# Kernel optimization log

Measured on AMD Instinct MI355X. Metric: run time of the kernel, lower is better.

Reference implementation:

```python
import jax, jax.numpy as jnp
import numpy as np

H, W = 480, 640
N = 256
CFEAT = 256
FAR = 80.0

def _quat_to_rot(q):
    # q: [N,4] normalized (w,x,y,z)
    w, x, y, z = q[:, 0], q[:, 1], q[:, 2], q[:, 3]
    return jnp.stack([
        jnp.stack([1 - 2 * (y * y + z * z), 2 * (x * y - w * z), 2 * (x * z + w * y)], -1),
        jnp.stack([2 * (x * y + w * z), 1 - 2 * (x * x + z * z), 2 * (y * z - w * x)], -1),
        jnp.stack([2 * (x * z - w * y), 2 * (y * z + w * x), 1 - 2 * (x * x + y * y)], -1)], -2)

def setup_inputs():
    key = jax.random.key(0)
    ks = jax.random.split(key, 10)
    z = jax.random.uniform(ks[0], (N,), minval=2.0, maxval=30.0)
    x = jax.random.uniform(ks[1], (N,), minval=-0.6, maxval=0.6) * z
    y = jax.random.uniform(ks[2], (N,), minval=-0.45, maxval=0.45) * z
    means3d = jnp.stack([x, y, z], -1)                                   # [N,3] in front of camera
    features = jax.random.normal(ks[3], (N, CFEAT))                      # [N,256]
    opacities = jax.random.uniform(ks[4], (N,), minval=0.3, maxval=0.95)
    scales = jax.random.uniform(ks[5], (N, 3), minval=0.05, maxval=0.4)
    rotations = jax.random.normal(ks[6], (N, 4))                         # unnormalized quats
    cam_K = jnp.array([[500.0, 0.0, 320.0], [0.0, 500.0, 240.0], [0.0, 0.0, 1.0]])
    cam_pose = jnp.eye(4)
    w1 = jax.random.normal(ks[7], (CFEAT, 128)) * (1.0 / np.sqrt(CFEAT))
    b1 = jnp.zeros((128,))
    w2 = jax.random.normal(ks[8], (128, 128)) * (1.0 / np.sqrt(128))
    b2 = jnp.zeros((128,))
    w3 = jax.random.normal(ks[9], (128, 12)) * (1.0 / np.sqrt(128))
    b3 = jnp.zeros((12,))
    return dict(means3d=means3d, features=features, opacities=opacities, scales=scales,
                rotations=rotations, cam_K=cam_K, cam_pose=cam_pose,
                w1=w1, b1=b1, w2=w2, b2=b2, w3=w3, b3=b3)

def _render(means3d, features, opacities, scales, rotations, cam_K, cam_pose):
    fx, fy = cam_K[0, 0], cam_K[1, 1]
    cx, cy = cam_K[0, 2], cam_K[1, 2]
    Rw, tw = cam_pose[:3, :3], cam_pose[:3, 3]
    tcam = means3d @ Rw.T + tw                                           # [N,3] camera-frame
    tz = tcam[:, 2]
    valid = tz > 0.01                                                    # near_plane cull
    tzs = jnp.where(valid, tz, 1.0)
    tx, ty = tcam[:, 0], tcam[:, 1]
    # 3D covariance: Sigma = R S S^T R^T
    q = rotations / (jnp.linalg.norm(rotations, axis=1, keepdims=True) + 1e-8)
    Rq = _quat_to_rot(q)                                                 # [N,3,3]
    M = Rq * scales[:, None, :]
    Sigma = jnp.einsum('nij,nkj->nik', M, M)
    Sc = jnp.einsum('ij,njk,lk->nil', Rw, Sigma, Rw)                     # world -> camera
    # EWA projection Jacobian [N,2,3]
    zero = jnp.zeros_like(tzs)
    J = jnp.stack([
        jnp.stack([fx / tzs, zero, -fx * tx / (tzs * tzs)], -1),
        jnp.stack([zero, fy / tzs, -fy * ty / (tzs * tzs)], -1)], -2)
    cov2d = jnp.einsum('nij,njk,nlk->nil', J, Sc, J) + 0.3 * jnp.eye(2)  # low-pass dilation
    a, b, c = cov2d[:, 0, 0], cov2d[:, 0, 1], cov2d[:, 1, 1]
    inv_det = 1.0 / jnp.maximum(a * c - b * b, 1e-12)
    A, B, C = c * inv_det, -b * inv_det, a * inv_det                     # conic
    u = fx * tx / tzs + cx
    v = fy * ty / tzs + cy
    px = jnp.arange(W, dtype=jnp.float32) + 0.5
    py = jnp.arange(H, dtype=jnp.float32) + 0.5
    dx = px[None, :] - u[:, None]                                        # [N,W]
    dy = py[None, :] - v[:, None]                                        # [N,H]
    power = (-(0.5 * A)[:, None, None] * (dx * dx)[:, None, :]
             - (0.5 * C)[:, None, None] * (dy * dy)[:, :, None]
             - B[:, None, None] * dy[:, :, None] * dx[:, None, :])       # [N,H,W]
    alpha = jnp.minimum(0.99, opacities[:, None, None] * jnp.exp(jnp.minimum(power, 0.0)))
    alpha = jnp.where(valid[:, None, None] & (alpha >= 1.0 / 255.0), alpha, 0.0)
    # front-to-back alpha compositing in depth order
    order = jnp.argsort(jnp.where(valid, tz, jnp.inf))
    alpha = jnp.take(alpha, order, axis=0).reshape(N, H * W)
    feats = jnp.take(features, order, axis=0)
    tzo = jnp.take(jnp.where(valid, tz, 0.0), order, axis=0)
    T = jnp.cumprod(1.0 - alpha, axis=0)
    T_excl = jnp.concatenate([jnp.ones((1, H * W), alpha.dtype), T[:-1]], axis=0)
    wgt = T_excl * alpha                                                 # [N,P]
    feat_img = jnp.einsum('np,nc->pc', wgt, feats).reshape(H, W, CFEAT)
    depth_img = jnp.einsum('np,n->p', wgt, tzo).reshape(H, W, 1)
    return feat_img, depth_img

def reference(means3d, features, opacities, scales, rotations, cam_K, cam_pose,
              w1, b1, w2, b2, w3, b3):
    rendered, depth = _render(means3d, features, opacities, scales, rotations, cam_K, cam_pose)
    depth = jnp.clip(depth, 0.0, FAR)
    h = jax.nn.relu(rendered @ w1 + b1)
    h = jax.nn.relu(h @ w2 + b2)
    seg = (h @ w3 + b3)[None]                                            # [1,H,W,12]
    return rendered, depth, seg
```

## Files before the change

### kernel.cpp

```cpp
#include <hip/hip_runtime.h>
#include <stdint.h>

#define HH 480
#define WW 640
#define NG 256
#define CF 256
#define FARV 80.0f
#define TILES_X (WW/64)
#define AST 264
#define BST 136

typedef __attribute__((ext_vector_type(4))) float f32x4;
typedef __attribute__((ext_vector_type(8))) short s16x8;

__device__ __forceinline__ unsigned short f2bf(float f){
  union { float f; unsigned int u; } c; c.f = f;
  unsigned int u = c.u + 0x7fffu + ((c.u >> 16) & 1u);
  return (unsigned short)(u >> 16);
}
__device__ __forceinline__ float bf2f(unsigned short h){
  union { unsigned int u; float f; } c; c.u = ((unsigned int)h) << 16; return c.f;
}

__global__ __launch_bounds__(256) void k_proj(
    const float* __restrict__ means3d,
    const float* __restrict__ opac,
    const float* __restrict__ scales,
    const float* __restrict__ rots,
    const float* __restrict__ camK,
    const float* __restrict__ camP,
    float* __restrict__ wspq,
    int* __restrict__ sidx)
{
  __shared__ float keys[NG];
  const int t = threadIdx.x;

  const float fx = camK[0], fy = camK[4];
  const float cx = camK[2], cy = camK[5];
  float Rw[3][3], tw[3];
#pragma unroll
  for (int r=0;r<3;r++){
#pragma unroll
    for (int c=0;c<3;c++) Rw[r][c] = camP[r*4+c];
    tw[r] = camP[r*4+3];
  }

  float mx = means3d[t*3+0], my = means3d[t*3+1], mz = means3d[t*3+2];
  float tcx = Rw[0][0]*mx + Rw[0][1]*my + Rw[0][2]*mz + tw[0];
  float tcy = Rw[1][0]*mx + Rw[1][1]*my + Rw[1][2]*mz + tw[1];
  float tcz = Rw[2][0]*mx + Rw[2][1]*my + Rw[2][2]*mz + tw[2];
  bool valid = tcz > 0.01f;
  float tzs = valid ? tcz : 1.0f;

  float qw = rots[t*4+0], qx = rots[t*4+1];
  float qy = rots[t*4+2], qz = rots[t*4+3];
  float nrm = sqrtf(qw*qw+qx*qx+qy*qy+qz*qz) + 1e-8f;
  qw /= nrm; qx /= nrm; qy /= nrm; qz /= nrm;
  float Rq[3][3];
  {
    float xx=qx*qx, yy=qy*qy, zz=qz*qz;
    float xy=qx*qy, xz=qx*qz, yz=qy*qz;
    float wx=qw*qx, wy=qw*qy, wz=qw*qz;
    Rq[0][0]=1.f-2.f*(yy+zz); Rq[0][1]=2.f*(xy-wz); Rq[0][2]=2.f*(xz+wy);
    Rq[1][0]=2.f*(xy+wz); Rq[1][1]=1.f-2.f*(xx+zz); Rq[1][2]=2.f*(yz-wx);
    Rq[2][0]=2.f*(xz-wy); Rq[2][1]=2.f*(yz+wx); Rq[2][2]=1.f-2.f*(xx+yy);
  }
  float s0 = scales[t*3+0], s1 = scales[t*3+1], s2 = scales[t*3+2];
  float s0s=s0*s0, s1s=s1*s1, s2s=s2*s2;
  float Sig[3][3];
#pragma unroll
  for (int i=0;i<3;i++)
#pragma unroll
    for (int j=0;j<3;j++)
      Sig[i][j] = s0s*Rq[i][0]*Rq[j][0] + s1s*Rq[i][1]*Rq[j][1] + s2s*Rq[i][2]*Rq[j][2];
  float Tm[3][3];
#pragma unroll
  for (int i=0;i<3;i++)
#pragma unroll
    for (int k=0;k<3;k++)
      Tm[i][k] = Rw[i][0]*Sig[0][k] + Rw[i][1]*Sig[1][k] + Rw[i][2]*Sig[2][k];
  float Sc[3][3];
#pragma unroll
  for (int i=0;i<3;i++)
#pragma unroll
    for (int l=0;l<3;l++)
      Sc[i][l] = Tm[i][0]*Rw[l][0] + Tm[i][1]*Rw[l][1] + Tm[i][2]*Rw[l][2];

  float iz = 1.0f / tzs;
  float r00 = fx*iz, r02 = -fx*tcx*iz*iz;
  float r11 = fy*iz, r12 = -fy*tcy*iz*iz;
  float v0 = Sc[0][0]*r00 + Sc[2][0]*r02;
  float v2 = Sc[0][2]*r00 + Sc[2][2]*r02;
  float v1 = Sc[0][1]*r00 + Sc[2][1]*r02;
  float a  = r00*v0 + r02*v2 + 0.3f;
  float bb = r11*v1 + r12*v2;
  float cc = r11*(Sc[1][1]*r11 + Sc[1][2]*r12) + r12*(Sc[2][1]*r11 + Sc[2][2]*r12) + 0.3f;
  float det = a*cc - bb*bb;
  float inv_det = 1.0f / fmaxf(det, 1e-12f);
  float Av = cc*inv_det, Bv = -bb*inv_det, Cv = a*inv_det;
  float u = fx*tcx*iz + cx;
  float v = fy*tcy*iz + cy;
  float op = opac[t];
  float op_eff = valid ? op : 0.0f;
  float tzo = valid ? tcz : 0.0f;
  float rx = -1.0f, ry = -1.0f;
  if (op_eff > (1.0f/255.0f)){
    float tau = logf(255.0f*op_eff);
    if (tau > 0.0f){
      rx = sqrtf(2.0f*tau*a) + 0.5f;
      ry = sqrtf(2.0f*tau*cc) + 0.5f;
    }
  }
  float key = valid ? tcz : __builtin_inff();

  keys[t] = key;
  __syncthreads();
  int rank = 0;
  for (int j=0;j<NG;j++){
    float kj = keys[j];
    rank += (kj < key) || (kj == key && j < t);
  }
  float4* wq = (float4*)wspq;
  float4 q0; q0.x = u;       q0.y = v;  q0.z = rx;       q0.w = ry;
  float4 q1; q1.x = 0.5f*Av; q1.y = Bv; q1.z = 0.5f*Cv;  q1.w = op_eff;
  float4 q2; q2.x = tzo;     q2.y = 0.f; q2.z = 0.f;     q2.w = 0.f;
  wq[rank*3+0] = q0;
  wq[rank*3+1] = q1;
  wq[rank*3+2] = q2;
  sidx[rank] = t;
}

__global__ __launch_bounds__(256) void k_gather(
    const float* __restrict__ features,
    const float* __restrict__ w1,
    const float* __restrict__ w2,
    const float* __restrict__ w3,
    const int* __restrict__ sidx,
    unsigned short* __restrict__ wsf,
    unsigned short* __restrict__ wt1,
    unsigned short* __restrict__ wt2,
    unsigned short* __restrict__ wt3)
{
  const int bx = blockIdx.x, t = threadIdx.x;
  if (bx < 64){
    int c = bx*256 + t;
    int row = c >> 6, c4 = c & 63;
    int src = sidx[row];
    float4 f = ((const float4*)features)[src*(CF/4) + c4];
    unsigned int* dst = (unsigned int*)(wsf + row*CF + c4*4);
    dst[0] = (unsigned)f2bf(f.x) | ((unsigned)f2bf(f.y) << 16);
    dst[1] = (unsigned)f2bf(f.z) | ((unsigned)f2bf(f.w) << 16);
  } else if (bx < 96){
    int base = (bx-64)*1024 + t*4;
#pragma unroll
    for (int e=0;e<4;e++){
      int d = base + e;
      int j = d >> 8, k = d & 255;
      wt1[d] = f2bf(w1[k*128 + j]);
    }
  } else if (bx < 104){
    int base = (bx-96)*2048 + t*8;
#pragma unroll
    for (int e=0;e<8;e++){
      int d = base + e;
      int j = d >> 7, k = d & 127;
      wt2[d] = f2bf(w2[k*128 + j]);
    }
  } else {
    int base = t*8;
#pragma unroll
    for (int e=0;e<8;e++){
      int d = base + e;
      int j = d >> 7, k = d & 127;
      wt3[d] = (j < 12) ? f2bf(w3[k*12 + j]) : (unsigned short)0;
    }
  }
}

__global__ __launch_bounds__(256) void k_fused(
    const float* __restrict__ wspq,
    const unsigned short* __restrict__ wsf,
    const unsigned short* __restrict__ wt1,
    const unsigned short* __restrict__ wt2,
    const unsigned short* __restrict__ wt3,
    const float* __restrict__ b1,
    const float* __restrict__ b2,
    const float* __restrict__ b3,
    float* __restrict__ out,
    float* __restrict__ dep,
    float* __restrict__ seg)
{
  __shared__ __align__(16) unsigned char smem[64*AST*2 + 17408 + 1296];
  unsigned short* sh_A = (unsigned short*)smem;
  unsigned char* X = smem + 64*AST*2;
  float* c_u    = (float*)X;
  float* c_v    = c_u + 256;
  float* c_hA   = c_u + 512;
  float* c_Bq   = c_u + 768;
  float* c_hC   = c_u + 1024;
  float* c_op   = c_u + 1280;
  float* c_tz   = c_u + 1536;
  float* chprod = c_u + 1792;
  unsigned short* stage = (unsigned short*)X;
  unsigned short* sh_B  = (unsigned short*)X;
  unsigned char* tail = smem + 64*AST*2 + 17408;
  float* depch = (float*)tail;
  unsigned char* act_idx = tail + 1024;
  int* wcnt = (int*)(tail + 1280);

  const int t = threadIdx.x;
  const int lane = t & 63;
  const int wvi = t >> 6;
  const int y  = blockIdx.x / TILES_X;
  const int x0 = (blockIdx.x % TILES_X) * 64;

  act_idx[t] = 0;
  const float4* wq = (const float4*)wspq;
  float4 q0 = wq[t*3+0];
  bool pred = (q0.z > 0.0f)
      && (q0.x + q0.z >= (float)x0 + 0.5f)
      && (q0.x - q0.z <= (float)x0 + 63.5f)
      && (fabsf(q0.y - ((float)y + 0.5f)) <= q0.w);
  unsigned long long m = __ballot(pred);
  if (lane == 0) wcnt[wvi] = __popcll(m);
  __syncthreads();
  int base = 0;
#pragma unroll
  for (int i=0;i<4;i++) base += (i < wvi) ? wcnt[i] : 0;
  const int nact = wcnt[0]+wcnt[1]+wcnt[2]+wcnt[3];
  if (pred){
    int pos = base + __popcll(m & ((1ull << lane) - 1ull));
    float4 q1 = wq[t*3+1];
    float4 q2 = wq[t*3+2];
    act_idx[pos] = (unsigned char)t;
    c_u[pos]  = q0.x;  c_v[pos]  = q0.y;
    c_hA[pos] = q1.x;  c_Bq[pos] = q1.y;  c_hC[pos] = q1.z;
    c_op[pos] = q1.w;  c_tz[pos] = q2.x;
  }
  __syncthreads();

  const int per8 = ((((nact + 3) >> 2) + 7) & ~7);
  const int n0 = wvi * per8;
  const int n1 = (nact < n0 + per8) ? nact : (n0 + per8);
  const float px = (float)(x0 + lane) + 0.5f;
  const float py = (float)y + 0.5f;

  const int ln  = lane & 15;
  const int kq8 = (lane >> 4) * 8;
  const int rq  = (lane >> 4) * 4;
  const int cb0 = wvi * 64;
  const int la = lane & 7, lb = lane >> 3;
  const int kchunks = (nact + 31) >> 5;

  uint4 cur[4], nxt[4];
  if (kchunks > 0){
#pragma unroll
    for (int g=0; g<4; g++){
      int kk = lb + 8*g;
      cur[g] = *(const uint4*)(wsf + (int)act_idx[kk]*CF + cb0 + la*8);
    }
  }

  {
    float prod = 1.0f;
    for (int ng = n0; ng < n0 + per8; ng += 8){
      union { unsigned short s[8]; uint4 v4; } alp;
#pragma unroll
      for (int e=0;e<8;e++){
        int n = ng + e;
        float al = 0.0f;
        if (n < n1){
          float dx = px - c_u[n], dy = py - c_v[n];
          float q = c_hA[n]*dx*dx + c_Bq[n]*dx*dy + c_hC[n]*dy*dy;
          al = fminf(0.99f, c_op[n]*__expf(fminf(-q, 0.0f)));
          if (al < (1.0f/255.0f)) al = 0.0f;
        }
        alp.s[e] = f2bf(al);
        prod *= 1.0f - bf2f(alp.s[e]);
      }
      *((uint4*)&sh_A[lane*AST + ng]) = alp.v4;
    }
    chprod[t] = prod;
  }
  __syncthreads();

  {
    float T = 1.0f;
#pragma unroll
    for (int c=0;c<4;c++) if (c < wvi) T *= chprod[c*64 + lane];
    float dacc = 0.0f;
    for (int ng = n0; ng < n0 + per8; ng += 8){
      union { unsigned short s[8]; uint4 v4; } ap, wp;
      ap.v4 = *((const uint4*)&sh_A[lane*AST + ng]);
#pragma unroll
      for (int e=0;e<8;e++){
        float al = bf2f(ap.s[e]);
        float wgt = T * al;
        T *= 1.0f - al;
        wp.s[e] = f2bf(wgt);
        int n = ng + e;
        if (n < n1) dacc += wgt * c_tz[n];
      }
      *((uint4*)&sh_A[lane*AST + ng]) = wp.v4;
    }
    depch[t] = dacc;
  }
  __syncthreads();

  unsigned short* stW = stage + wvi*2048;
  const int xw = (la & 3) << 3;

  f32x4 acc[4][4];
#pragma unroll
  for (int mt=0;mt<4;mt++)
#pragma unroll
    for (int nt=0;nt<4;nt++){
      f32x4 z = {0.f,0.f,0.f,0.f};
      acc[mt][nt] = z;
    }
  for (int kb=0; kb<kchunks; kb++){
#pragma unroll
    for (int g=0; g<4; g++){
      const unsigned short* s = (const unsigned short*)&cur[g];
      int colw = (lb + 8*g) ^ xw;
#pragma unroll
      for (int i=0;i<8;i++)
        stW[(la*8 + i)*32 + colw] = s[i];
    }
    if (kb+1 < kchunks){
#pragma unroll
      for (int g=0; g<4; g++){
        int kk = (kb+1)*32 + lb + 8*g;
        nxt[g] = *(const uint4*)(wsf + (int)act_idx[kk]*CF + cb0 + la*8);
      }
    }
    int k0 = kb*32;
    s16x8 bfr[4];
#pragma unroll
    for (int nt=0;nt<4;nt++){
      int chl = nt*16 + ln;
      int colr = kq8 ^ (((chl >> 3) & 3) << 3);
      bfr[nt] = *(const s16x8*)(stW + chl*32 + colr);
    }
#pragma unroll
    for (int mt=0;mt<4;mt++){
      s16x8 afr = *(const s16x8*)(&sh_A[(mt*16 + ln)*AST + k0 + kq8]);
#pragma unroll
      for (int nt=0;nt<4;nt++)
        acc[mt][nt] = __builtin_amdgcn_mfma_f32_16x16x32_bf16(afr, bfr[nt], acc[mt][nt], 0, 0, 0);
    }
    if (kb+1 < kchunks){
#pragma unroll
      for (int g=0; g<4; g++) cur[g] = nxt[g];
    }
  }
  __syncthreads();

#pragma unroll
  for (int mt=0;mt<4;mt++)
#pragma unroll
    for (int nt=0;nt<4;nt++)
#pragma unroll
      for (int r=0;r<4;r++){
        int row = mt*16 + rq + r;
        int col = cb0 + nt*16 + ln;
        sh_A[row*AST + col] = f2bf(acc[mt][nt][r]);
      }
  __syncthreads();

  const int n0m = wvi * 32;
  f32x4 acc1[4][2];
#pragma unroll
  for (int nn=0;nn<2;nn++){
    float bv = b1[n0m + nn*16 + ln];
    f32x4 b4 = {bv,bv,bv,bv};
#pragma unroll
    for (int mt=0;mt<4;mt++) acc1[mt][nn] = b4;
  }
#pragma unroll
  for (int k0=0;k0<256;k0+=32){
    s16x8 bfr0 = *(const s16x8*)(wt1 + (n0m + 0*16 + ln)*256 + k0 + kq8);
    s16x8 bfr1 = *(const s16x8*)(wt1 + (n0m + 1*16 + ln)*256 + k0 + kq8);
#pragma unroll
    for (int mt=0;mt<4;mt++){
      s16x8 afr = *(const s16x8*)(&sh_A[(mt*16 + ln)*AST + k0 + kq8]);
      acc1[mt][0] = __builtin_amdgcn_mfma_f32_16x16x32_bf16(afr, bfr0, acc1[mt][0], 0, 0, 0);
      acc1[mt][1] = __builtin_amdgcn_mfma_f32_16x16x32_bf16(afr, bfr1, acc1[mt][1], 0, 0, 0);
    }
  }
#pragma unroll
  for (int mt=0;mt<4;mt++)
#pragma unroll
    for (int nn=0;nn<2;nn++)
#pragma unroll
      for (int r=0;r<4;r++){
        int mrow = mt*16 + rq + r;
        int ncol = n0m + nn*16 + ln;
        sh_B[mrow*BST + ncol] = f2bf(fmaxf(acc1[mt][nn][r], 0.0f));
      }
  __syncthreads();

  f32x4 acc2[4][2];
#pragma unroll
  for (int nn=0;nn<2;nn++){
    float bv = b2[n0m + nn*16 + ln];
    f32x4 b4 = {bv,bv,bv,bv};
#pragma unroll
    for (int mt=0;mt<4;mt++) acc2[mt][nn] = b4;
  }
#pragma unroll
  for (int k0=0;k0<128;k0+=32){
    s16x8 bfr0 = *(const s16x8*)(wt2 + (n0m + 0*16 + ln)*128 + k0 + kq8);
    s16x8 bfr1 = *(const s16x8*)(wt2 + (n0m + 1*16 + ln)*128 + k0 + kq8);
#pragma unroll
    for (int mt=0;mt<4;mt++){
      s16x8 afr = *(const s16x8*)(&sh_B[(mt*16 + ln)*BST + k0 + kq8]);
      acc2[mt][0] = __builtin_amdgcn_mfma_f32_16x16x32_bf16(afr, bfr0, acc2[mt][0], 0, 0, 0);
      acc2[mt][1] = __builtin_amdgcn_mfma_f32_16x16x32_bf16(afr, bfr1, acc2[mt][1], 0, 0, 0);
    }
  }
  __syncthreads();
#pragma unroll
  for (int mt=0;mt<4;mt++)
#pragma unroll
    for (int nn=0;nn<2;nn++)
#pragma unroll
      for (int r=0;r<4;r++){
        int mrow = mt*16 + rq + r;
        int ncol = n0m + nn*16 + ln;
        sh_B[mrow*BST + ncol] = f2bf(fmaxf(acc2[mt][nn][r], 0.0f));
      }
  __syncthreads();

  const size_t Pbase = (size_t)(y*WW + x0);
  f32x4 acc3;
  {
    float bv = (ln < 12) ? b3[ln] : 0.0f;
    f32x4 b4 = {bv,bv,bv,bv};
    acc3 = b4;
  }
#pragma unroll
  for (int k0=0;k0<128;k0+=32){
    s16x8 afr = *(const s16x8*)(&sh_B[(wvi*16 + ln)*BST + k0 + kq8]);
    s16x8 bfr = *(const s16x8*)(wt3 + ln*128 + k0 + kq8);
    acc3 = __builtin_amdgcn_mfma_f32_16x16x32_bf16(afr, bfr, acc3, 0, 0, 0);
  }
  if (ln < 12){
#pragma unroll
    for (int r=0;r<4;r++){
      int mrow = wvi*16 + rq + r;
      seg[(Pbase + mrow)*12 + ln] = acc3[r];
    }
  }

  if (wvi == 0){
    float d = depch[lane] + depch[64+lane] + depch[128+lane] + depch[192+lane];
    dep[y*WW + x0 + lane] = fminf(fmaxf(d, 0.0f), FARV);
  }

  {
    const int pxb = wvi*16;
    for (int i=0;i<16;i++){
      int pix = pxb + i;
      uint2 dv = *(const uint2*)(&sh_A[pix*AST + lane*4]);
      f32x4 o;
      o[0] = bf2f((unsigned short)(dv.x & 0xffffu));
      o[1] = bf2f((unsigned short)(dv.x >> 16));
      o[2] = bf2f((unsigned short)(dv.y & 0xffffu));
      o[3] = bf2f((unsigned short)(dv.y >> 16));
      __builtin_nontemporal_store(o, (f32x4*)(&out[(Pbase + pix)*CF + lane*4]));
    }
  }
}

extern "C" void kernel_launch(void* const* d_in, const int* in_sizes, int n_in,
                              void* d_out, int out_size, void* d_ws, size_t ws_size,
                              hipStream_t stream) {
  (void)in_sizes; (void)n_in; (void)out_size; (void)ws_size;
  const float* means3d  = (const float*)d_in[0];
  const float* features = (const float*)d_in[1];
  const float* opac     = (const float*)d_in[2];
  const float* scales   = (const float*)d_in[3];
  const float* rots     = (const float*)d_in[4];
  const float* camK     = (const float*)d_in[5];
  const float* camP     = (const float*)d_in[6];
  const float* w1       = (const float*)d_in[7];
  const float* b1       = (const float*)d_in[8];
  const float* w2       = (const float*)d_in[9];
  const float* b2       = (const float*)d_in[10];
  const float* w3       = (const float*)d_in[11];
  const float* b3       = (const float*)d_in[12];

  char* ws = (char*)d_ws;
  float*          wspq = (float*)ws;
  int*            sidx = (int*)(ws + 12288);
  unsigned short* wsf  = (unsigned short*)(ws + 13312);
  unsigned short* wt1  = (unsigned short*)(ws + 144384);
  unsigned short* wt2  = (unsigned short*)(ws + 209920);
  unsigned short* wt3  = (unsigned short*)(ws + 242688);

  float* out = (float*)d_out;
  float* dep = out + (size_t)HH*WW*CF;
  float* seg = dep + (size_t)HH*WW;

  k_proj<<<1, 256, 0, stream>>>(means3d, opac, scales, rots, camK, camP, wspq, sidx);
  k_gather<<<105, 256, 0, stream>>>(features, w1, w2, w3, sidx, wsf, wt1, wt2, wt3);
  k_fused<<<HH*TILES_X, 256, 0, stream>>>(wspq, wsf, wt1, wt2, wt3, b1, b2, b3, out, dep, seg);
}
```

Before: 112.8 us.

## Precompute per-Gaussian first MLP layer and fuse into compositing GEMM

Uses linearity of the first MLP layer: features@w1 is precomputed per Gaussian in the gather kernel, and the per-pixel layer-1 activations are accumulated as weights times this projected table inside the existing compositing K-loop. This removes the separate 256-deep layer-1 GEMM over rendered features and a barrier, replacing it with extra MFMAs proportional to the active Gaussian count. It adds per-iteration LDS staging of the projected rows and changes rounding, since the projection is stored in bf16.

```diff
diff --git a/kernel.cpp b/kernel.cpp
--- a/kernel.cpp
+++ b/kernel.cpp
@@ -137,7 +137,7 @@
     const float* __restrict__ w3,
     const int* __restrict__ sidx,
     unsigned short* __restrict__ wsf,
-    unsigned short* __restrict__ wt1,
+    unsigned short* __restrict__ wsg1,
     unsigned short* __restrict__ wt2,
     unsigned short* __restrict__ wt3)
 {
@@ -150,23 +150,15 @@
     unsigned int* dst = (unsigned int*)(wsf + row*CF + c4*4);
     dst[0] = (unsigned)f2bf(f.x) | ((unsigned)f2bf(f.y) << 16);
     dst[1] = (unsigned)f2bf(f.z) | ((unsigned)f2bf(f.w) << 16);
-  } else if (bx < 96){
-    int base = (bx-64)*1024 + t*4;
-#pragma unroll
-    for (int e=0;e<4;e++){
-      int d = base + e;
-      int j = d >> 8, k = d & 255;
-      wt1[d] = f2bf(w1[k*128 + j]);
-    }
-  } else if (bx < 104){
-    int base = (bx-96)*2048 + t*8;
+  } else if (bx < 72){
+    int base = (bx-64)*2048 + t*8;
 #pragma unroll
     for (int e=0;e<8;e++){
       int d = base + e;
       int j = d >> 7, k = d & 127;
       wt2[d] = f2bf(w2[k*128 + j]);
     }
-  } else {
+  } else if (bx < 73){
     int base = t*8;
 #pragma unroll
     for (int e=0;e<8;e++){
@@ -174,13 +166,25 @@
       int j = d >> 7, k = d & 127;
       wt3[d] = (j < 12) ? f2bf(w3[k*12 + j]) : (unsigned short)0;
     }
+  } else {
+    __shared__ float frow[CF];
+    int g = bx - 73;
+    int src = sidx[g];
+    if (t < 64) ((float4*)frow)[t] = ((const float4*)features)[src*(CF/4) + t];
+    __syncthreads();
+    if (t < 128){
+      float s = 0.0f;
+      for (int k=0;k<CF;k++)
+        s += frow[k] * w1[k*128 + t];
+      wsg1[g*128 + t] = f2bf(s);
+    }
   }
 }
 
 __global__ __launch_bounds__(256) void k_fused(
     const float* __restrict__ wspq,
     const unsigned short* __restrict__ wsf,
-    const unsigned short* __restrict__ wt1,
+    const unsigned short* __restrict__ wsg1,
     const unsigned short* __restrict__ wt2,
     const unsigned short* __restrict__ wt3,
     const float* __restrict__ b1,
@@ -250,7 +254,9 @@
   const int rq  = (lane >> 4) * 4;
   const int cb0 = wvi * 64;
   const int la = lane & 7, lb = lane >> 3;
+  const int rG = lane >> 1, hcG = lane & 1;
   const int kchunks = (nact + 31) >> 5;
+  const int n0m = wvi * 32;
 
   uint4 cur[4], nxt[4];
   if (kchunks > 0){
@@ -318,7 +324,17 @@
       f32x4 z = {0.f,0.f,0.f,0.f};
       acc[mt][nt] = z;
     }
+  f32x4 acc1[4][2];
+#pragma unroll
+  for (int nn=0;nn<2;nn++){
+    float bv = b1[n0m + nn*16 + ln];
+    f32x4 b4 = {bv,bv,bv,bv};
+#pragma unroll
+    for (int mt=0;mt<4;mt++) acc1[mt][nn] = b4;
+  }
+
   for (int kb=0; kb<kchunks; kb++){
+    int k0 = kb*32;
 #pragma unroll
     for (int g=0; g<4; g++){
       const unsigned short* s = (const unsigned short*)&cur[g];
@@ -334,7 +350,10 @@
         nxt[g] = *(const uint4*)(wsf + (int)act_idx[kk]*CF + cb0 + la*8);
       }
     }
-    int k0 = kb*32;
+    s16x8 afr[4];
+#pragma unroll
+    for (int mt=0;mt<4;mt++)
+      afr[mt] = *(const s16x8*)(&sh_A[(mt*16 + ln)*AST + k0 + kq8]);
     s16x8 bfr[4];
 #pragma unroll
     for (int nt=0;nt<4;nt++){
@@ -343,12 +362,32 @@
       bfr[nt] = *(const s16x8*)(stW + chl*32 + colr);
     }
 #pragma unroll
-    for (int mt=0;mt<4;mt++){
-      s16x8 afr = *(const s16x8*)(&sh_A[(mt*16 + ln)*AST + k0 + kq8]);
+    for (int mt=0;mt<4;mt++)
 #pragma unroll
       for (int nt=0;nt<4;nt++)
-        acc[mt][nt] = __builtin_amdgcn_mfma_f32_16x16x32_bf16(afr, bfr[nt], acc[mt][nt], 0, 0, 0);
-    }
+        acc[mt][nt] = __builtin_amdgcn_mfma_f32_16x16x32_bf16(afr[mt], bfr[nt], acc[mt][nt], 0, 0, 0);
+    {
+      const unsigned short* gsrc = wsg1 + (int)act_idx[k0 + rG]*128 + n0m + hcG*16;
+      uint4 ga = *(const uint4*)gsrc;
+      uint4 gb = *(const uint4*)(gsrc + 8);
+      const unsigned short* gap = (const unsigned short*)&ga;
+      const unsigned short* gbp = (const unsigned short*)&gb;
+#pragma unroll
+      for (int c2=0;c2<8;c2++)
+        stW[(hcG*16 + c2)*40 + rG] = gap[c2];
+#pragma unroll
+      for (int c2=0;c2<8;c2++)
+        stW[(hcG*16 + 8 + c2)*40 + rG] = gbp[c2];
+    }
+    s16x8 bfrG[2];
+#pragma unroll
+    for (int nt2=0;nt2<2;nt2++)
+      bfrG[nt2] = *(const s16x8*)(stW + (nt2*16 + ln)*40 + kq8);
+#pragma unroll
+    for (int mt=0;mt<4;mt++)
+#pragma unroll
+      for (int nt2=0;nt2<2;nt2++)
+        acc1[mt][nt2] = __builtin_amdgcn_mfma_f32_16x16x32_bf16(afr[mt], bfrG[nt2], acc1[mt][nt2], 0, 0, 0);
     if (kb+1 < kchunks){
 #pragma unroll
       for (int g=0; g<4; g++) cur[g] = nxt[g];
@@ -366,28 +405,6 @@
         int col = cb0 + nt*16 + ln;
         sh_A[row*AST + col] = f2bf(acc[mt][nt][r]);
       }
-  __syncthreads();
-
-  const int n0m = wvi * 32;
-  f32x4 acc1[4][2];
-#pragma unroll
-  for (int nn=0;nn<2;nn++){
-    float bv = b1[n0m + nn*16 + ln];
-    f32x4 b4 = {bv,bv,bv,bv};
-#pragma unroll
-    for (int mt=0;mt<4;mt++) acc1[mt][nn] = b4;
-  }
-#pragma unroll
-  for (int k0=0;k0<256;k0+=32){
-    s16x8 bfr0 = *(const s16x8*)(wt1 + (n0m + 0*16 + ln)*256 + k0 + kq8);
-    s16x8 bfr1 = *(const s16x8*)(wt1 + (n0m + 1*16 + ln)*256 + k0 + kq8);
-#pragma unroll
-    for (int mt=0;mt<4;mt++){
-      s16x8 afr = *(const s16x8*)(&sh_A[(mt*16 + ln)*AST + k0 + kq8]);
-      acc1[mt][0] = __builtin_amdgcn_mfma_f32_16x16x32_bf16(afr, bfr0, acc1[mt][0], 0, 0, 0);
-      acc1[mt][1] = __builtin_amdgcn_mfma_f32_16x16x32_bf16(afr, bfr1, acc1[mt][1], 0, 0, 0);
-    }
-  }
 #pragma unroll
   for (int mt=0;mt<4;mt++)
 #pragma unroll
@@ -495,7 +512,7 @@
   float*          wspq = (float*)ws;
   int*            sidx = (int*)(ws + 12288);
   unsigned short* wsf  = (unsigned short*)(ws + 13312);
-  unsigned short* wt1  = (unsigned short*)(ws + 144384);
+  unsigned short* wsg1 = (unsigned short*)(ws + 144384);
   unsigned short* wt2  = (unsigned short*)(ws + 209920);
   unsigned short* wt3  = (unsigned short*)(ws + 242688);
 
@@ -504,6 +521,6 @@
   float* seg = dep + (size_t)HH*WW;
 
   k_proj<<<1, 256, 0, stream>>>(means3d, opac, scales, rots, camK, camP, wspq, sidx);
-  k_gather<<<105, 256, 0, stream>>>(features, w1, w2, w3, sidx, wsf, wt1, wt2, wt3);
-  k_fused<<<HH*TILES_X, 256, 0, stream>>>(wspq, wsf, wt1, wt2, wt3, b1, b2, b3, out, dep, seg);
+  k_gather<<<329, 256, 0, stream>>>(features, w1, w2, w3, sidx, wsf, wsg1, wt2, wt3);
+  k_fused<<<HH*TILES_X, 256, 0, stream>>>(wspq, wsf, wsg1, wt2, wt3, b1, b2, b3, out, dep, seg);
 }
```

Result: no change. 114.2 us (+1.3%).
